# Kernel optimization log

Measured on AMD Instinct MI355X. Metric: run time of the kernel, lower is better.

## Reference

```python
import jax, jax.numpy as jnp
import numpy as np

MARGIN = 0.3
NORM = 2.0  # p-norm used by both pairwise() and PairwiseDistance

M, C = 65536, 256   # n*h*w pixels, feature channels
K, P, Q = 20, 2048, 2048  # classes 1..nclass-1, positives, negatives per class


def setup_inputs() -> dict:
    key = jax.random.key(0)
    k1, k2, k3 = jax.random.split(key, 3)
    features = jax.random.normal(k1, (M, C), dtype=jnp.float32)
    pos_idx = jax.random.randint(k2, (K, P), 0, M)
    neg_idx = jax.random.randint(k3, (K, Q), 0, M)
    return {"features": features, "pos_idx": pos_idx, "neg_idx": neg_idx}


def _pairwise(x, y):
    # torch: clamp(xx - 2xy + yy, 0); (dis + eps) ** (1/norm)
    eps = 0.0001 / x.shape[1]
    xx = jnp.sum(x * x, axis=1)           # [P]
    yy = jnp.sum(y * y, axis=1)           # [Q]
    xy = x @ y.T                           # [P,Q] GEMM
    dis = jnp.clip(xx[:, None] - 2.0 * xy + yy[None, :], 0.0)
    return (dis + eps) ** (1.0 / NORM)


def _pdist(x1, x2):
    # PairwiseDistance: (clamp(sum(|x1-x2|^p), 0) + eps) ** (1/p)
    eps = 0.0001 / x1.shape[1]
    out = jnp.sum(jnp.abs(x1 - x2) ** NORM, axis=1)
    return (jnp.clip(out, 0.0) + eps) ** (1.0 / NORM)


def _class_loss(pos, neg):
    # hard mining on detached features (indices only, as in generate_triplet_simple)
    pos_d = jax.lax.stop_gradient(pos)
    neg_d = jax.lax.stop_gradient(neg)
    hp = jnp.argmax(_pairwise(pos_d, pos_d), axis=1)   # hardest positive per anchor
    hn = jnp.argmin(_pairwise(pos_d, neg_d), axis=1)   # hardest negative per anchor
    d_p = _pdist(pos, pos[hp])
    d_n = _pdist(pos, neg[hn])
    return jnp.mean(jnp.clip(MARGIN + d_p - d_n, 0.0))


def reference(features, pos_idx, neg_idx):
    f = jax.nn.sigmoid(features)          # torch.sigmoid(features)
    pos = f[pos_idx]                      # [K,P,C]
    neg = f[neg_idx]                      # [K,Q,C]
    losses = jax.vmap(_class_loss)(pos, neg)  # per-class triplet losses
    return jnp.sum(losses)                # loss accumulated over classes
```

## Files before the change

### kernel.cpp

```cpp
#include <hip/hip_runtime.h>
#include <stdint.h>

#define M_ROWS 65536
#define C_DIM  256
#define K_CLS  20
#define P_POS  2048
#define MARGIN_F 0.3f
#define EPS_D (0.0001f / 256.0f)
#define SCALE1 0x7F7F7F7Fu
#define SCALE2 0x80808080u

typedef float floatx4 __attribute__((ext_vector_type(4)));
typedef int   intx8   __attribute__((ext_vector_type(8)));
union Frag8 { intx8 v; uint4 q[2]; };

__device__ __forceinline__ void async_copy16(const void* g, void* l) {
    __builtin_amdgcn_global_load_lds(
        (const __attribute__((address_space(1))) void*)g,
        (__attribute__((address_space(3))) void*)l, 16, 0, 0);
}
__device__ __forceinline__ float sigm(float x) { return 1.f / (1.f + __expf(-x)); }

__device__ __forceinline__ void negA(Frag8& f) {
#pragma unroll
    for (int t = 0; t < 8; ++t) f.v[t] ^= (int)0x80808080u;
}

#define VMCNT2() asm volatile("s_waitcnt vmcnt(2)" ::: "memory")
#define VMCNT0() asm volatile("s_waitcnt vmcnt(0)" ::: "memory")

__global__ __launch_bounds__(256) void sigmoid_norm_k(
        const float* __restrict__ feat,
        unsigned int* __restrict__ S8,
        float* __restrict__ xx,
        unsigned int* __restrict__ hp,
        unsigned int* __restrict__ hn) {
    {
        const int idx = blockIdx.x * 256 + threadIdx.x;
        if (idx < K_CLS * P_POS) { hp[idx] = 0u; hn[idx] = 0xFFFFFFFFu; }
    }
    const int wave = threadIdx.x >> 6, lane = threadIdx.x & 63;
    const int row = blockIdx.x * 4 + wave;
    const float4 v = *(const float4*)(feat + (size_t)row * C_DIM + lane * 4);

    const int p01 = __builtin_amdgcn_cvt_pk_fp8_f32(sigm(v.x), sigm(v.y), 0, false);
    const int p23 = __builtin_amdgcn_cvt_pk_fp8_f32(sigm(v.z), sigm(v.w), 0, false);
    const unsigned int packed = (unsigned int)(p01 & 0xFFFF) | ((unsigned int)p23 << 16);
    S8[(size_t)row * 64 + lane] = packed;

    const float q0 = __builtin_amdgcn_cvt_f32_fp8(p01, 0);
    const float q1 = __builtin_amdgcn_cvt_f32_fp8(p01, 1);
    const float q2 = __builtin_amdgcn_cvt_f32_fp8(p23, 0);
    const float q3 = __builtin_amdgcn_cvt_f32_fp8(p23, 1);
    float sum = q0 * q0 + q1 * q1 + q2 * q2 + q3 * q3;
#pragma unroll
    for (int off = 32; off; off >>= 1) sum += __shfl_down(sum, off);
    if (lane == 0) xx[row] = sum;
}

__global__ __launch_bounds__(256, 3) void select_k(
        const unsigned int* __restrict__ S8,
        const float* __restrict__ xx,
        const int* __restrict__ pos_idx,
        const int* __restrict__ neg_idx,
        unsigned int* __restrict__ hp,
        unsigned int* __restrict__ hn) {
    __shared__ __align__(16) unsigned char Bt[3][32 * 256];
    __shared__ float yyL[512];

    const int tid    = threadIdx.x;
    const int w      = tid >> 6;
    const int lane   = tid & 63;
    const int lane15 = lane & 15;
    const int quad   = lane >> 4;

    const int bid    = blockIdx.x;
    const int ctid   = bid % 40;
    const int rest   = bid / 40;
    const int i_blk  = rest >> 2;
    const int jq     = rest & 3;
    const int k      = ctid >> 1;
    const int isNeg  = ctid & 1;
    const int i0     = i_blk * 256;
    const int j0     = jq * 512;

    const int* __restrict__ idxA = pos_idx + k * P_POS;
    const int* __restrict__ idxB = (isNeg ? neg_idx : pos_idx) + k * P_POS;
    unsigned int* outKey         = (isNeg ? hn : hp) + k * P_POS;

    const char* S8B = (const char*)S8;

    const int rl  = lane >> 4;
    const int cch = lane & 15;
    int rloc[2], soff[2];
#pragma unroll
    for (int c = 0; c < 2; ++c) {
        rloc[c] = (w * 2 + c) * 4 + rl;
        soff[c] = (cch ^ (rloc[c] & 15)) << 4;
    }

    uint32_t g_pk[16];
#pragma unroll
    for (int t = 0; t < 16; ++t) {
        const uint32_t a0 = (uint32_t)idxB[j0 + t * 32 + rloc[0]];
        const uint32_t a1 = (uint32_t)idxB[j0 + t * 32 + rloc[1]];
        g_pk[t] = (a0 & 0xFFFFu) | (a1 << 16);
    }

#pragma unroll
    for (int t = 0; t < 2; ++t) {
        const int jj = t * 256 + tid;
        yyL[jj] = xx[idxB[j0 + jj]];
    }

    Frag8 A_reg[4][2];
#pragma unroll
    for (int si = 0; si < 4; ++si) {
        const int gi = idxA[i0 + w * 64 + si * 16 + lane15];
        const char* rb = S8B + ((size_t)(uint32_t)gi << 8) + quad * 32;
#pragma unroll
        for (int s = 0; s < 2; ++s) {
            A_reg[si][s].q[0] = *(const uint4*)(rb + s * 128);
            A_reg[si][s].q[1] = *(const uint4*)(rb + s * 128 + 16);
            negA(A_reg[si][s]);
        }
    }

    int blo[2], bhi[2];
#pragma unroll
    for (int s = 0; s < 2; ++s) {
        const int c0 = s * 8 + quad * 2;
        blo[s] = lane15 * 256 + ((c0 ^ lane15) << 4);
        bhi[s] = lane15 * 256 + (((c0 + 1) ^ lane15) << 4);
    }

#pragma unroll
    for (int t = 0; t < 2; ++t) {
        char* lb = (char*)&Bt[t][0] + (w * 2) * 1024;
        async_copy16(S8B + ((size_t)(g_pk[t] & 0xFFFFu) << 8) + soff[0], lb);
        async_copy16(S8B + ((size_t)(g_pk[t] >> 16) << 8) + soff[1], lb + 1024);
    }

    float bestv[16];
    const float binit = isNeg ? 3.4e38f : -3.4e38f;
#pragma unroll
    for (int t = 0; t < 16; ++t) bestv[t] = binit;

    __syncthreads();

#pragma unroll
    for (int jc = 0; jc < 16; ++jc) {
        if (jc) {
            if (jc == 15) VMCNT0(); else VMCNT2();
            __builtin_amdgcn_s_barrier();
            __builtin_amdgcn_sched_barrier(0);
        }

        const float yv0 = yyL[(jc << 5) + lane15];
        const float yv1 = yyL[(jc << 5) + 16 + lane15];

        if (jc < 14) {
            const uint32_t pk = g_pk[jc + 2];
            char* lb = (char*)&Bt[(jc + 2) % 3][0] + (w * 2) * 1024;
            async_copy16(S8B + ((size_t)(pk & 0xFFFFu) << 8) + soff[0], lb);
            async_copy16(S8B + ((size_t)(pk >> 16) << 8) + soff[1], lb + 1024);
        }

        const char* Bb = (const char*)&Bt[jc % 3][0];
        const floatx4 yv4_0 = {yv0, yv0, yv0, yv0};
        const floatx4 yv4_1 = {yv1, yv1, yv1, yv1};
        floatx4 acc[2][4];
        {
            Frag8 bf0, bf1;
            bf0.q[0] = *(const uint4*)(Bb + blo[0]);
            bf0.q[1] = *(const uint4*)(Bb + bhi[0]);
            bf1.q[0] = *(const uint4*)(Bb + blo[0] + 4096);
            bf1.q[1] = *(const uint4*)(Bb + bhi[0] + 4096);
#pragma unroll
            for (int si = 0; si < 4; ++si)
                acc[0][si] = __builtin_amdgcn_mfma_scale_f32_16x16x128_f8f6f4(
                    A_reg[si][0].v, bf0.v, yv4_0, 0, 0,
                    0, SCALE2, 0, SCALE1);
#pragma unroll
            for (int si = 0; si < 4; ++si)
                acc[1][si] = __builtin_amdgcn_mfma_scale_f32_16x16x128_f8f6f4(
                    A_reg[si][0].v, bf1.v, yv4_1, 0, 0,
                    0, SCALE2, 0, SCALE1);
        }
        {
            Frag8 bf0, bf1;
            bf0.q[0] = *(const uint4*)(Bb + blo[1]);
            bf0.q[1] = *(const uint4*)(Bb + bhi[1]);
            bf1.q[0] = *(const uint4*)(Bb + blo[1] + 4096);
            bf1.q[1] = *(const uint4*)(Bb + bhi[1] + 4096);
#pragma unroll
            for (int si = 0; si < 4; ++si)
                acc[0][si] = __builtin_amdgcn_mfma_scale_f32_16x16x128_f8f6f4(
                    A_reg[si][1].v, bf0.v, acc[0][si], 0, 0,
                    0, SCALE2, 0, SCALE1);
#pragma unroll
            for (int si = 0; si < 4; ++si)
                acc[1][si] = __builtin_amdgcn_mfma_scale_f32_16x16x128_f8f6f4(
                    A_reg[si][1].v, bf1.v, acc[1][si], 0, 0,
                    0, SCALE2, 0, SCALE1);
        }

        const uint32_t jb0 = (uint32_t)((j0 + (jc << 5)) | lane15);
        const uint32_t jb1 = jb0 | 16u;
#pragma unroll
        for (int si = 0; si < 4; ++si)
#pragma unroll
            for (int r = 0; r < 4; ++r) {
                const float e0 = __uint_as_float(
                    (__float_as_uint(acc[0][si][r]) & 0xFFFFF800u) | jb0);
                const float e1 = __uint_as_float(
                    (__float_as_uint(acc[1][si][r]) & 0xFFFFF800u) | jb1);
                const int slot = si * 4 + r;
                bestv[slot] = isNeg ? fminf(fminf(bestv[slot], e0), e1)
                                    : fmaxf(fmaxf(bestv[slot], e0), e1);
            }
    }

#pragma unroll
    for (int slot = 0; slot < 16; ++slot) {
#pragma unroll
        for (int off = 1; off < 16; off <<= 1) {
            const float ov = __shfl_xor(bestv[slot], off);
            bestv[slot] = isNeg ? fminf(bestv[slot], ov) : fmaxf(bestv[slot], ov);
        }
    }
    if (lane15 == 0) {
#pragma unroll
        for (int si = 0; si < 4; ++si)
#pragma unroll
            for (int r = 0; r < 4; ++r) {
                const int row = w * 64 + si * 16 + quad * 4 + r;
                const uint32_t u = __float_as_uint(bestv[si * 4 + r]);
                const uint32_t key = (u & 0x80000000u) ? ~u : (u | 0x80000000u);
                if (isNeg) atomicMin(&outKey[i0 + row], key);
                else       atomicMax(&outKey[i0 + row], key);
            }
    }
}

#define ACC16(UA, UP, UN)                                                     \
    {                                                                         \
        float xa, d;                                                          \
        xa = __builtin_amdgcn_cvt_f32_fp8((int)(UA), 0);                      \
        d = xa - __builtin_amdgcn_cvt_f32_fp8((int)(UP), 0); dp += d * d;     \
        d = xa - __builtin_amdgcn_cvt_f32_fp8((int)(UN), 0); dn += d * d;     \
        xa = __builtin_amdgcn_cvt_f32_fp8((int)(UA), 1);                      \
        d = xa - __builtin_amdgcn_cvt_f32_fp8((int)(UP), 1); dp += d * d;     \
        d = xa - __builtin_amdgcn_cvt_f32_fp8((int)(UN), 1); dn += d * d;     \
        xa = __builtin_amdgcn_cvt_f32_fp8((int)(UA), 2);                      \
        d = xa - __builtin_amdgcn_cvt_f32_fp8((int)(UP), 2); dp += d * d;     \
        d = xa - __builtin_amdgcn_cvt_f32_fp8((int)(UN), 2); dn += d * d;     \
        xa = __builtin_amdgcn_cvt_f32_fp8((int)(UA), 3);                      \
        d = xa - __builtin_amdgcn_cvt_f32_fp8((int)(UP), 3); dp += d * d;     \
        d = xa - __builtin_amdgcn_cvt_f32_fp8((int)(UN), 3); dn += d * d;     \
    }

__global__ __launch_bounds__(256) void loss_k(
        const unsigned int* __restrict__ S8,
        const int* __restrict__ pos_idx,
        const int* __restrict__ neg_idx,
        const unsigned int* __restrict__ hp,
        const unsigned int* __restrict__ hn,
        float* __restrict__ terms) {
    const int tid    = threadIdx.x;
    const int lane15 = tid & 15;
    const int grp    = tid >> 4;
    const int a      = blockIdx.x * 16 + grp;
    const int k      = a >> 11;
    const int i      = a & 2047;
    const int* pidx = pos_idx + (k << 11);
    const int* nidx = neg_idx + (k << 11);
    const unsigned int kp = hp[a], kn = hn[a];
    const int jp = (int)((kp & 0x80000000u) ? (kp & 2047u) : ((~kp) & 2047u));
    const int jn = (int)((kn & 0x80000000u) ? (kn & 2047u) : ((~kn) & 2047u));
    const int ga = pidx[i];
    const int gp = pidx[jp];
    const int gn = nidx[jn];

    const char* S8B = (const char*)S8;
    const uint4 va = *(const uint4*)(S8B + ((size_t)(uint32_t)ga << 8) + lane15 * 16);
    const uint4 vp = *(const uint4*)(S8B + ((size_t)(uint32_t)gp << 8) + lane15 * 16);
    const uint4 vn = *(const uint4*)(S8B + ((size_t)(uint32_t)gn << 8) + lane15 * 16);

    float dp = 0.f, dn = 0.f;
    ACC16(va.x, vp.x, vn.x)
    ACC16(va.y, vp.y, vn.y)
    ACC16(va.z, vp.z, vn.z)
    ACC16(va.w, vp.w, vn.w)

#pragma unroll
    for (int off = 1; off < 16; off <<= 1) {
        dp += __shfl_xor(dp, off);
        dn += __shfl_xor(dn, off);
    }
    if (lane15 == 0) {
        const float d_p = sqrtf(fmaxf(dp, 0.f) + EPS_D);
        const float d_n = sqrtf(fmaxf(dn, 0.f) + EPS_D);
        terms[a] = fmaxf(MARGIN_F + d_p - d_n, 0.f);
    }
}

__global__ __launch_bounds__(1024) void reduce_k(
        const float* __restrict__ terms, float* __restrict__ out) {
    __shared__ float red[1024];
    float s = 0.f;
    for (int i = threadIdx.x; i < K_CLS * P_POS; i += 1024) s += terms[i];
    red[threadIdx.x] = s;
    __syncthreads();
    for (int off = 512; off; off >>= 1) {
        if ((int)threadIdx.x < off) red[threadIdx.x] += red[threadIdx.x + off];
        __syncthreads();
    }
    if (threadIdx.x == 0) out[0] = red[0] * (1.0f / (float)P_POS);
}

extern "C" void kernel_launch(void* const* d_in, const int* in_sizes, int n_in,
                              void* d_out, int out_size, void* d_ws, size_t ws_size,
                              hipStream_t stream) {
    const float* feat    = (const float*)d_in[0];
    const int*   pos_idx = (const int*)d_in[1];
    const int*   neg_idx = (const int*)d_in[2];

    char* ws = (char*)d_ws;
    unsigned int* S8 = (unsigned int*)ws;
    float*        xx = (float*)(ws + 16777216);
    unsigned int* hp = (unsigned int*)(ws + 17039360);
    unsigned int* hn = (unsigned int*)(ws + 17203200);
    float*     terms = (float*)(ws + 17367040);

    sigmoid_norm_k<<<M_ROWS / 4, 256, 0, stream>>>(feat, S8, xx, hp, hn);

    select_k<<<32 * 40, 256, 0, stream>>>(S8, xx, pos_idx, neg_idx, hp, hn);

    loss_k<<<(K_CLS * P_POS) / 16, 256, 0, stream>>>(S8, pos_idx, neg_idx, hp, hn, terms);

    reduce_k<<<1, 1024, 0, stream>>>(terms, (float*)d_out);
}
```

Baseline: 168.9 us.

## Deepen select_k prefetch to six LDS buffers and fuse final reduction via atomics

```diff
diff --git a/kernel.cpp b/kernel.cpp
--- a/kernel.cpp
+++ b/kernel.cpp
@@ -26,7 +26,7 @@
     for (int t = 0; t < 8; ++t) f.v[t] ^= (int)0x80808080u;
 }
 
-#define VMCNT2() asm volatile("s_waitcnt vmcnt(2)" ::: "memory")
+#define VMCNT4() asm volatile("s_waitcnt vmcnt(4)" ::: "memory")
 #define VMCNT0() asm volatile("s_waitcnt vmcnt(0)" ::: "memory")
 
 __global__ __launch_bounds__(256) void sigmoid_norm_k(
@@ -34,10 +34,12 @@
         unsigned int* __restrict__ S8,
         float* __restrict__ xx,
         unsigned int* __restrict__ hp,
-        unsigned int* __restrict__ hn) {
+        unsigned int* __restrict__ hn,
+        float* __restrict__ out) {
     {
         const int idx = blockIdx.x * 256 + threadIdx.x;
         if (idx < K_CLS * P_POS) { hp[idx] = 0u; hn[idx] = 0xFFFFFFFFu; }
+        if (idx == 0) out[0] = 0.f;
     }
     const int wave = threadIdx.x >> 6, lane = threadIdx.x & 63;
     const int row = blockIdx.x * 4 + wave;
@@ -65,7 +67,7 @@
         const int* __restrict__ neg_idx,
         unsigned int* __restrict__ hp,
         unsigned int* __restrict__ hn) {
-    __shared__ __align__(16) unsigned char Bt[3][32 * 256];
+    __shared__ __align__(16) unsigned char Bt[6][32 * 256];
     __shared__ float yyL[512];
 
     const int tid    = threadIdx.x;
@@ -134,91 +136,99 @@
         bhi[s] = lane15 * 256 + (((c0 + 1) ^ lane15) << 4);
     }
 
-#pragma unroll
-    for (int t = 0; t < 2; ++t) {
+    float bestv[16];
+    const float binit = isNeg ? 3.4e38f : -3.4e38f;
+#pragma unroll
+    for (int t = 0; t < 16; ++t) bestv[t] = binit;
+
+    __syncthreads();
+
+#pragma unroll
+    for (int t = 0; t < 4; ++t) {
         char* lb = (char*)&Bt[t][0] + (w * 2) * 1024;
         async_copy16(S8B + ((size_t)(g_pk[t] & 0xFFFFu) << 8) + soff[0], lb);
         async_copy16(S8B + ((size_t)(g_pk[t] >> 16) << 8) + soff[1], lb + 1024);
     }
 
-    float bestv[16];
-    const float binit = isNeg ? 3.4e38f : -3.4e38f;
-#pragma unroll
-    for (int t = 0; t < 16; ++t) bestv[t] = binit;
-
-    __syncthreads();
-
-#pragma unroll
-    for (int jc = 0; jc < 16; ++jc) {
-        if (jc) {
-            if (jc == 15) VMCNT0(); else VMCNT2();
-            __builtin_amdgcn_s_barrier();
-            __builtin_amdgcn_sched_barrier(0);
+#pragma unroll
+    for (int p = 0; p < 8; ++p) {
+        if (p == 7) VMCNT0(); else VMCNT4();
+        __builtin_amdgcn_s_barrier();
+        __builtin_amdgcn_sched_barrier(0);
+
+        if (p < 6) {
+#pragma unroll
+            for (int u = 0; u < 2; ++u) {
+                const int t = 2 * p + 4 + u;
+                const uint32_t pk = g_pk[t];
+                char* lb = (char*)&Bt[t % 6][0] + (w * 2) * 1024;
+                async_copy16(S8B + ((size_t)(pk & 0xFFFFu) << 8) + soff[0], lb);
+                async_copy16(S8B + ((size_t)(pk >> 16) << 8) + soff[1], lb + 1024);
+            }
         }
 
-        const float yv0 = yyL[(jc << 5) + lane15];
-        const float yv1 = yyL[(jc << 5) + 16 + lane15];
-
-        if (jc < 14) {
-            const uint32_t pk = g_pk[jc + 2];
-            char* lb = (char*)&Bt[(jc + 2) % 3][0] + (w * 2) * 1024;
-            async_copy16(S8B + ((size_t)(pk & 0xFFFFu) << 8) + soff[0], lb);
-            async_copy16(S8B + ((size_t)(pk >> 16) << 8) + soff[1], lb + 1024);
+#pragma unroll
+        for (int u = 0; u < 2; ++u) {
+            const int jc = 2 * p + u;
+            const char* Bb = (const char*)&Bt[jc % 6][0];
+            const float yv0 = yyL[(jc << 5) + lane15];
+            const float yv1 = yyL[(jc << 5) + 16 + lane15];
+            const floatx4 yv4_0 = {yv0, yv0, yv0, yv0};
+            const floatx4 yv4_1 = {yv1, yv1, yv1, yv1};
+            floatx4 acc[2][4];
+
+            __builtin_amdgcn_s_setprio(1);
+            {
+                Frag8 bf0, bf1;
+                bf0.q[0] = *(const uint4*)(Bb + blo[0]);
+                bf0.q[1] = *(const uint4*)(Bb + bhi[0]);
+                bf1.q[0] = *(const uint4*)(Bb + blo[0] + 4096);
+                bf1.q[1] = *(const uint4*)(Bb + bhi[0] + 4096);
+#pragma unroll
+                for (int si = 0; si < 4; ++si)
+                    acc[0][si] = __builtin_amdgcn_mfma_scale_f32_16x16x128_f8f6f4(
+                        A_reg[si][0].v, bf0.v, yv4_0, 0, 0,
+                        0, SCALE2, 0, SCALE1);
+#pragma unroll
+                for (int si = 0; si < 4; ++si)
+                    acc[1][si] = __builtin_amdgcn_mfma_scale_f32_16x16x128_f8f6f4(
+                        A_reg[si][0].v, bf1.v, yv4_1, 0, 0,
+                        0, SCALE2, 0, SCALE1);
+            }
+            {
+                Frag8 bf0, bf1;
+                bf0.q[0] = *(const uint4*)(Bb + blo[1]);
+                bf0.q[1] = *(const uint4*)(Bb + bhi[1]);
+                bf1.q[0] = *(const uint4*)(Bb + blo[1] + 4096);
+                bf1.q[1] = *(const uint4*)(Bb + bhi[1] + 4096);
+#pragma unroll
+                for (int si = 0; si < 4; ++si)
+                    acc[0][si] = __builtin_amdgcn_mfma_scale_f32_16x16x128_f8f6f4(
+                        A_reg[si][1].v, bf0.v, acc[0][si], 0, 0,
+                        0, SCALE2, 0, SCALE1);
+#pragma unroll
+                for (int si = 0; si < 4; ++si)
+                    acc[1][si] = __builtin_amdgcn_mfma_scale_f32_16x16x128_f8f6f4(
+                        A_reg[si][1].v, bf1.v, acc[1][si], 0, 0,
+                        0, SCALE2, 0, SCALE1);
+            }
+            __builtin_amdgcn_s_setprio(0);
+
+            const uint32_t jb0 = (uint32_t)((j0 + (jc << 5)) | lane15);
+            const uint32_t jb1 = jb0 | 16u;
+#pragma unroll
+            for (int si = 0; si < 4; ++si)
+#pragma unroll
+                for (int r = 0; r < 4; ++r) {
+                    const float e0 = __uint_as_float(
+                        (__float_as_uint(acc[0][si][r]) & 0xFFFFF800u) | jb0);
+                    const float e1 = __uint_as_float(
+                        (__float_as_uint(acc[1][si][r]) & 0xFFFFF800u) | jb1);
+                    const int slot = si * 4 + r;
+                    bestv[slot] = isNeg ? fminf(fminf(bestv[slot], e0), e1)
+                                        : fmaxf(fmaxf(bestv[slot], e0), e1);
+                }
         }
-
-        const char* Bb = (const char*)&Bt[jc % 3][0];
-        const floatx4 yv4_0 = {yv0, yv0, yv0, yv0};
-        const floatx4 yv4_1 = {yv1, yv1, yv1, yv1};
-        floatx4 acc[2][4];
-        {
-            Frag8 bf0, bf1;
-            bf0.q[0] = *(const uint4*)(Bb + blo[0]);
-            bf0.q[1] = *(const uint4*)(Bb + bhi[0]);
-            bf1.q[0] = *(const uint4*)(Bb + blo[0] + 4096);
-            bf1.q[1] = *(const uint4*)(Bb + bhi[0] + 4096);
-#pragma unroll
-            for (int si = 0; si < 4; ++si)
-                acc[0][si] = __builtin_amdgcn_mfma_scale_f32_16x16x128_f8f6f4(
-                    A_reg[si][0].v, bf0.v, yv4_0, 0, 0,
-                    0, SCALE2, 0, SCALE1);
-#pragma unroll
-            for (int si = 0; si < 4; ++si)
-                acc[1][si] = __builtin_amdgcn_mfma_scale_f32_16x16x128_f8f6f4(
-                    A_reg[si][0].v, bf1.v, yv4_1, 0, 0,
-                    0, SCALE2, 0, SCALE1);
-        }
-        {
-            Frag8 bf0, bf1;
-            bf0.q[0] = *(const uint4*)(Bb + blo[1]);
-            bf0.q[1] = *(const uint4*)(Bb + bhi[1]);
-            bf1.q[0] = *(const uint4*)(Bb + blo[1] + 4096);
-            bf1.q[1] = *(const uint4*)(Bb + bhi[1] + 4096);
-#pragma unroll
-            for (int si = 0; si < 4; ++si)
-                acc[0][si] = __builtin_amdgcn_mfma_scale_f32_16x16x128_f8f6f4(
-                    A_reg[si][1].v, bf0.v, acc[0][si], 0, 0,
-                    0, SCALE2, 0, SCALE1);
-#pragma unroll
-            for (int si = 0; si < 4; ++si)
-                acc[1][si] = __builtin_amdgcn_mfma_scale_f32_16x16x128_f8f6f4(
-                    A_reg[si][1].v, bf1.v, acc[1][si], 0, 0,
-                    0, SCALE2, 0, SCALE1);
-        }
-
-        const uint32_t jb0 = (uint32_t)((j0 + (jc << 5)) | lane15);
-        const uint32_t jb1 = jb0 | 16u;
-#pragma unroll
-        for (int si = 0; si < 4; ++si)
-#pragma unroll
-            for (int r = 0; r < 4; ++r) {
-                const float e0 = __uint_as_float(
-                    (__float_as_uint(acc[0][si][r]) & 0xFFFFF800u) | jb0);
-                const float e1 = __uint_as_float(
-                    (__float_as_uint(acc[1][si][r]) & 0xFFFFF800u) | jb1);
-                const int slot = si * 4 + r;
-                bestv[slot] = isNeg ? fminf(fminf(bestv[slot], e0), e1)
-                                    : fmaxf(fmaxf(bestv[slot], e0), e1);
-            }
     }
 
 #pragma unroll
@@ -266,7 +276,8 @@
         const int* __restrict__ neg_idx,
         const unsigned int* __restrict__ hp,
         const unsigned int* __restrict__ hn,
-        float* __restrict__ terms) {
+        float* __restrict__ out) {
+    __shared__ float sm[16];
     const int tid    = threadIdx.x;
     const int lane15 = tid & 15;
     const int grp    = tid >> 4;
@@ -301,22 +312,15 @@
     if (lane15 == 0) {
         const float d_p = sqrtf(fmaxf(dp, 0.f) + EPS_D);
         const float d_n = sqrtf(fmaxf(dn, 0.f) + EPS_D);
-        terms[a] = fmaxf(MARGIN_F + d_p - d_n, 0.f);
-    }
-}
-
-__global__ __launch_bounds__(1024) void reduce_k(
-        const float* __restrict__ terms, float* __restrict__ out) {
-    __shared__ float red[1024];
-    float s = 0.f;
-    for (int i = threadIdx.x; i < K_CLS * P_POS; i += 1024) s += terms[i];
-    red[threadIdx.x] = s;
+        sm[grp] = fmaxf(MARGIN_F + d_p - d_n, 0.f);
+    }
     __syncthreads();
-    for (int off = 512; off; off >>= 1) {
-        if ((int)threadIdx.x < off) red[threadIdx.x] += red[threadIdx.x + off];
-        __syncthreads();
-    }
-    if (threadIdx.x == 0) out[0] = red[0] * (1.0f / (float)P_POS);
+    if (tid == 0) {
+        float s = 0.f;
+#pragma unroll
+        for (int g = 0; g < 16; ++g) s += sm[g];
+        atomicAdd(out, s * (1.0f / (float)P_POS));
+    }
 }
 
 extern "C" void kernel_launch(void* const* d_in, const int* in_sizes, int n_in,
@@ -331,13 +335,12 @@
     float*        xx = (float*)(ws + 16777216);
     unsigned int* hp = (unsigned int*)(ws + 17039360);
     unsigned int* hn = (unsigned int*)(ws + 17203200);
-    float*     terms = (float*)(ws + 17367040);
-
-    sigmoid_norm_k<<<M_ROWS / 4, 256, 0, stream>>>(feat, S8, xx, hp, hn);
+
+    sigmoid_norm_k<<<M_ROWS / 4, 256, 0, stream>>>(feat, S8, xx, hp, hn,
+                                                   (float*)d_out);
 
     select_k<<<32 * 40, 256, 0, stream>>>(S8, xx, pos_idx, neg_idx, hp, hn);
 
-    loss_k<<<(K_CLS * P_POS) / 16, 256, 0, stream>>>(S8, pos_idx, neg_idx, hp, hn, terms);
-
-    reduce_k<<<1, 1024, 0, stream>>>(terms, (float*)d_out);
-}
+    loss_k<<<(K_CLS * P_POS) / 16, 256, 0, stream>>>(S8, pos_idx, neg_idx, hp, hn,
+                                                     (float*)d_out);
+}
```

After: 188.7 us. +11.7%, slower.
